# Kernel optimization log

Hardware: AMD Instinct MI355X
Metric: run time of the kernel (lower is better)

The kernel has to match this reference:

```python
import jax, jax.numpy as jnp
import numpy as np

B, T, E, H, V = 256, 32, 512, 512, 3000
SKIP = 2


def setup_inputs() -> dict:
    key = jax.random.key(0)
    ks = jax.random.split(key, 12)
    # sorted-descending ragged lengths, max forced to T (pack_padded_sequence requires descending)
    lengths = np.sort(np.asarray(jax.random.randint(ks[0], (B,), T // 2, T + 1)))[::-1].copy()
    lengths[0] = T
    s = 0.05
    return {
        "image_features": jax.random.normal(ks[1], (B, E // 2), jnp.float32),
        "text_features": jax.random.normal(ks[2], (B, E // 2), jnp.float32),
        "h0": jnp.zeros((B, H), jnp.float32),
        "c0": jnp.zeros((B, H), jnp.float32),
        "embed_table": jax.random.normal(ks[3], (V, E), jnp.float32) * 0.02,
        "W_ih": jax.random.normal(ks[4], (4 * H, E), jnp.float32) * s,
        "W_hh": jax.random.normal(ks[5], (4 * H, H), jnp.float32) * s,
        "b_ih": jnp.zeros((4 * H,), jnp.float32),
        "b_hh": jnp.zeros((4 * H,), jnp.float32),
        "W_out": jax.random.normal(ks[6], (V, 2 * H), jnp.float32) * s,
        "b_out": jnp.zeros((V,), jnp.float32),
        "answer": jax.random.randint(ks[7], (B, T), 0, V),
        "answer_lengths": lengths,  # numpy int array (static)
    }


def _lstm_cell(x, hx, cx, W_ih, W_hh, b_ih, b_hh):
    # torch.nn.LSTMCell math: gates ordered i, f, g, o
    g = x @ W_ih.T + b_ih + hx @ W_hh.T + b_hh
    i, f, gg, o = jnp.split(g, 4, axis=-1)
    cy = jax.nn.sigmoid(f) * cx + jax.nn.sigmoid(i) * jnp.tanh(gg)
    hy = jax.nn.sigmoid(o) * jnp.tanh(cy)
    return hy, cy


def _packed_indices(lengths, max_len, batch):
    # torch pack_padded_sequence (batch_first) ordering: for each timestep t,
    # rows 0..batch_sizes[t] of the (descending-sorted) batch, time-major concat.
    lengths = np.asarray(lengths)
    idx = np.concatenate([t * batch + np.arange(int((lengths > t).sum())) for t in range(max_len)])
    return jnp.asarray(idx)


def reference(image_features, text_features, h0, c0, embed_table,
              W_ih, W_hh, b_ih, b_hh, W_out, b_out, answer, answer_lengths):
    batch = image_features.shape[0]
    max_len = int(np.max(np.asarray(answer_lengths)))
    combined = jnp.concatenate([image_features, text_features], axis=1)  # [B, E]
    emb = embed_table[answer]                                            # [B, T, E]
    # inputs over time: step 0 = combined, steps 1..max_len-1 = embedded answer tokens
    xs = jnp.concatenate([combined[:, None, :], emb[:, : max_len - 1, :]], axis=1)
    xs = jnp.transpose(xs, (1, 0, 2))                                    # [T, B, E]
    ts = jnp.arange(max_len)

    def step(carry, inp):
        hx, cx, h_m2, h_m1, c_m2, c_m1 = carry
        t, x = inp
        hy, cy = _lstm_cell(x, hx, cx, W_ih, W_hh, b_ih, b_hh)
        # periodic skip-state residual: applied to the carried state AFTER storing hy/cy
        cond = (t >= SKIP) & (t % (SKIP + 1) == 0)
        hx_n = jnp.where(cond, hy + h_m2, hy)
        cx_n = jnp.where(cond, cy + c_m2, cy)
        return (hx_n, cx_n, h_m1, hy, c_m1, cy), (hy, cy)

    z = jnp.zeros_like(h0)
    (_, _, _, _, _, _), (hs, cs) = jax.lax.scan(step, (h0, c0, z, z, z, z), (ts, xs))
    results = jnp.concatenate([hs, cs], axis=-1)          # [T, B, 2H], time-major
    flat = results.reshape(max_len * batch, 2 * results.shape[-1] // 2)
    idx = _packed_indices(answer_lengths, max_len, batch)
    packed = flat[idx]                                    # [sum(lengths), 2H]
    return packed @ W_out.T + b_out                       # [sum(lengths), V]
```

## Files before the change

kernel.cpp:

```cpp
#include <hip/hip_runtime.h>
#include <hip/hip_bf16.h>

#define T_STEPS 32
#define BATCH 256
#define EDIM 512
#define HDIM 512
#define G4 2048
#define VOCAB 3000
#define VPAD 3072

#define NB_CVTW   8192
#define NB_WOUT   12288
#define NB_XS     16384
#define NB_CARRY  512

typedef short bf16x8 __attribute__((ext_vector_type(8)));
typedef float f32x4 __attribute__((ext_vector_type(4)));

__device__ __forceinline__ unsigned short f2b(float f){
  union { float f; unsigned int u; } x; x.f = f;
  unsigned int u = x.u;
  unsigned int r = (u + 0x7fffu + ((u >> 16) & 1u)) >> 16;
  return (unsigned short)r;
}
__device__ __forceinline__ float b2f(unsigned short h){
  union { unsigned int u; float f; } x; x.u = ((unsigned int)h) << 16;
  return x.f;
}
__device__ __forceinline__ float sigm(float x){ return 1.0f / (1.0f + expf(-x)); }

__device__ __forceinline__ void gload_lds16(const unsigned short* g, unsigned short* l){
  __builtin_amdgcn_global_load_lds(
      (const __attribute__((address_space(1))) unsigned int*)g,
      (__attribute__((address_space(3))) unsigned int*)l, 16, 0, 0);
}

__global__ __launch_bounds__(256) void k_prep(
    const float* __restrict__ wih, const float* __restrict__ whh,
    const float* __restrict__ wout,
    const float* __restrict__ img, const float* __restrict__ txt,
    const float* __restrict__ emb, const int* __restrict__ ans,
    const float* __restrict__ h0, const float* __restrict__ c0,
    const int* __restrict__ lengths,
    unsigned short* __restrict__ o_ih, unsigned short* __restrict__ o_hh,
    unsigned short* __restrict__ o_wo, unsigned short* __restrict__ xs,
    unsigned short* __restrict__ hx, float* __restrict__ cx,
    int* __restrict__ bs, int* __restrict__ roff, int* __restrict__ meta,
    int* __restrict__ rmap){
  int bid = blockIdx.x;
  if (bid < NB_CVTW){
    int i = bid * 256 + threadIdx.x;
    int n1 = G4 * EDIM;
    if (i < n1) o_ih[i] = f2b(wih[i]);
    else o_hh[i - n1] = f2b(whh[i - n1]);
    return;
  }
  bid -= NB_CVTW;
  if (bid < NB_WOUT){
    int i = bid * 256 + threadIdx.x;
    int r = i >> 10, c = i & 1023;
    o_wo[i] = (r < VOCAB) ? f2b(wout[r * 1024 + c]) : (unsigned short)0;
    return;
  }
  bid -= NB_WOUT;
  if (bid < NB_XS){
    int i = bid * 256 + threadIdx.x;
    int e = i & (EDIM - 1);
    int r = i >> 9;
    int t = r >> 8, b = r & 255;
    float v;
    if (t == 0) v = (e < 256) ? img[b * 256 + e] : txt[b * 256 + (e - 256)];
    else { int tok = ans[b * T_STEPS + (t - 1)]; v = emb[(size_t)tok * EDIM + e]; }
    xs[i] = f2b(v);
    return;
  }
  bid -= NB_XS;
  if (bid < NB_CARRY){
    int i = bid * 256 + threadIdx.x;
    hx[i] = f2b(h0[i]); cx[i] = c0[i];
    return;
  }
  {
    __shared__ int s[T_STEPS];
    __shared__ int sroff[T_STEPS + 1];
    int t = threadIdx.x;
    if (t < T_STEPS){
      int c = 0;
      for (int i = 0; i < BATCH; i++) c += (lengths[i] > t) ? 1 : 0;
      s[t] = c; bs[t] = c;
    }
    __syncthreads();
    if (t == 0){
      int acc = 0;
      for (int u = 0; u < T_STEPS; u++){ sroff[u] = acc; roff[u] = acc; acc += s[u]; }
      sroff[T_STEPS] = acc;
      meta[0] = acc;
    }
    __syncthreads();
    int ntot = sroff[T_STEPS];
    for (int r = t; r < T_STEPS * BATCH; r += 256){
      int tt = r >> 8, b = r & 255;
      if (b < s[tt]) rmap[sroff[tt] + b] = r;
    }
    for (int r = ntot + t; r < T_STEPS * BATCH; r += 256) rmap[r] = -1;
  }
}

template<int K>
__device__ __forceinline__ void gemm_tile(const unsigned short* __restrict__ A,
                                          const unsigned short* __restrict__ B,
                                          int row0, int col0,
                                          unsigned short* As, unsigned short* Bs,
                                          f32x4 acc[4][4]){
  const int tid = threadIdx.x, w = tid >> 6, l = tid & 63;
  const int la = l & 15, lkq = l >> 4;
  const int sr = l >> 3;
  const int ss = (l & 7) ^ sr;
  const int wr = (w >> 1) * 64, wc = (w & 1) * 64;
  const unsigned short* gA = A + (size_t)(row0 + w * 32 + sr) * K + ss * 8;
  const unsigned short* gB = B + (size_t)(col0 + w * 32 + sr) * K + ss * 8;
  unsigned short* lA = As + (w * 32) * 64;
  unsigned short* lB = Bs + (w * 32) * 64;
  for (int k0 = 0; k0 < K; k0 += 64){
#pragma unroll
    for (int i = 0; i < 4; i++){
      gload_lds16(gA + (size_t)i * 8 * K + k0, lA + i * 8 * 64);
      gload_lds16(gB + (size_t)i * 8 * K + k0, lB + i * 8 * 64);
    }
    __syncthreads();
#pragma unroll
    for (int kk = 0; kk < 2; kk++){
      bf16x8 a[4], b[4];
#pragma unroll
      for (int i = 0; i < 4; i++){
        int r = wr + i * 16 + la;
        a[i] = *(const bf16x8*)(As + r * 64 + (((kk * 4 + lkq) ^ (r & 7)) << 3));
      }
#pragma unroll
      for (int i = 0; i < 4; i++){
        int r = wc + i * 16 + la;
        b[i] = *(const bf16x8*)(Bs + r * 64 + (((kk * 4 + lkq) ^ (r & 7)) << 3));
      }
#pragma unroll
      for (int mi = 0; mi < 4; mi++)
#pragma unroll
        for (int ni = 0; ni < 4; ni++)
          acc[mi][ni] = __builtin_amdgcn_mfma_f32_16x16x32_bf16(a[mi], b[ni], acc[mi][ni], 0, 0, 0);
    }
    __syncthreads();
  }
}

__global__ __launch_bounds__(256) void k_gemm_xw(const unsigned short* __restrict__ A,
                                                 const unsigned short* __restrict__ W,
                                                 const float* __restrict__ bih,
                                                 const float* __restrict__ bhh,
                                                 unsigned short* __restrict__ C){
  __shared__ unsigned short As[128 * 64], Bs[128 * 64];
  int row0 = blockIdx.x * 128, col0 = blockIdx.y * 128;
  f32x4 acc[4][4] = {};
  gemm_tile<EDIM>(A, W, row0, col0, As, Bs, acc);
  int tid = threadIdx.x, w = tid >> 6, l = tid & 63;
  int la = l & 15, r4 = (l >> 4) * 4;
  int wr = (w >> 1) * 64, wc = (w & 1) * 64;
#pragma unroll
  for (int ni = 0; ni < 4; ni++){
    int col = col0 + wc + ni * 16 + la;
    float bias = bih[col] + bhh[col];
#pragma unroll
    for (int mi = 0; mi < 4; mi++)
#pragma unroll
      for (int j = 0; j < 4; j++){
        int row = row0 + wr + mi * 16 + r4 + j;
        C[(size_t)row * G4 + col] = f2b(acc[mi][ni][j] + bias);
      }
  }
}

__global__ __launch_bounds__(256, 2) void k_lstm_step(
    const unsigned short* __restrict__ XWt,
    const unsigned short* __restrict__ Whh,
    const unsigned short* __restrict__ hin,
    unsigned short* __restrict__ hout,
    float* __restrict__ cxio,
    unsigned short* __restrict__ hs_t,
    unsigned short* __restrict__ cs_t,
    const unsigned short* __restrict__ hs_m2,
    const unsigned short* __restrict__ cs_m2,
    int do_res){
  __shared__ unsigned short hA[16 * 512];
  __shared__ float gbuf[4][16][17];
  const int w = threadIdx.x >> 6, l = threadIdx.x & 63;
  const int la = l & 15, lkq = l >> 4;
  const int row0 = blockIdx.x * 16;
  const int hc0  = blockIdx.y * 16;
#pragma unroll
  for (int i = 0; i < 4; i++){
    int r = i * 4 + w;
    gload_lds16(hin + (size_t)(row0 + r) * HDIM + ((l ^ (r & 7)) << 3), hA + r * 512);
  }
  const unsigned short* Bp = Whh + (size_t)(w * HDIM + hc0 + la) * HDIM + lkq * 8;
  bf16x8 b[16];
#pragma unroll
  for (int kk = 0; kk < 16; kk++) b[kk] = *(const bf16x8*)(Bp + kk * 32);
  const int r4 = lkq * 4;
  float x[4];
#pragma unroll
  for (int j = 0; j < 4; j++)
    x[j] = b2f(XWt[(size_t)(row0 + r4 + j) * G4 + w * HDIM + hc0 + la]);
  __syncthreads();
  f32x4 acc = {};
#pragma unroll
  for (int kk = 0; kk < 16; kk++){
    bf16x8 a = *(const bf16x8*)(hA + la * 512 + (((kk * 4 + lkq) ^ (la & 7)) << 3));
    acc = __builtin_amdgcn_mfma_f32_16x16x32_bf16(a, b[kk], acc, 0, 0, 0);
  }
#pragma unroll
  for (int j = 0; j < 4; j++) gbuf[w][r4 + j][la] = acc[j] + x[j];
  __syncthreads();
  {
    int r = threadIdx.x >> 4, c = threadIdx.x & 15;
    size_t p = (size_t)(row0 + r) * HDIM + hc0 + c;
    float gi = gbuf[0][r][c], gf = gbuf[1][r][c], gg = gbuf[2][r][c], go = gbuf[3][r][c];
    float cprev = cxio[p];
    float cy = sigm(gf) * cprev + sigm(gi) * tanhf(gg);
    float hy = sigm(go) * tanhf(cy);
    hs_t[p] = f2b(hy);
    cs_t[p] = f2b(cy);
    float hn = hy, cn = cy;
    if (do_res){ hn += b2f(hs_m2[p]); cn += b2f(cs_m2[p]); }
    hout[p] = f2b(hn);
    cxio[p] = cn;
  }
}

__global__ __launch_bounds__(256) void k_gemm_out(const unsigned short* __restrict__ hs,
                                                  const unsigned short* __restrict__ cs,
                                                  const unsigned short* __restrict__ Wo,
                                                  const float* __restrict__ bout,
                                                  const int* __restrict__ meta,
                                                  const int* __restrict__ rmap,
                                                  float* __restrict__ out){
  int ntot = meta[0];
  int row0 = blockIdx.x * 128, col0 = blockIdx.y * 128;
  if (row0 >= ntot) return;
  __shared__ unsigned short As[128 * 64], Bs[128 * 64];
  const int tid = threadIdx.x, w = tid >> 6, l = tid & 63;
  const int la = l & 15, lkq = l >> 4;
  const int sr = l >> 3, ss = (l & 7) ^ sr;
  const int wr = (w >> 1) * 64, wc = (w & 1) * 64;
  int srow[4];
#pragma unroll
  for (int i = 0; i < 4; i++){
    int rr = rmap[row0 + w * 32 + sr + i * 8];
    srow[i] = rr < 0 ? 0 : rr;
  }
  const unsigned short* gB = Wo + (size_t)(col0 + w * 32 + sr) * 1024 + ss * 8;
  unsigned short* lA = As + (w * 32) * 64;
  unsigned short* lB = Bs + (w * 32) * 64;
  f32x4 acc[4][4] = {};
  for (int k0 = 0; k0 < 1024; k0 += 64){
#pragma unroll
    for (int i = 0; i < 4; i++){
      const unsigned short* srcA = (k0 < 512)
          ? hs + (size_t)srow[i] * 512 + k0 + ss * 8
          : cs + (size_t)srow[i] * 512 + (k0 - 512) + ss * 8;
      gload_lds16(srcA, lA + i * 8 * 64);
      gload_lds16(gB + (size_t)i * 8 * 1024 + k0, lB + i * 8 * 64);
    }
    __syncthreads();
#pragma unroll
    for (int kk = 0; kk < 2; kk++){
      bf16x8 a[4], b[4];
#pragma unroll
      for (int i = 0; i < 4; i++){
        int r = wr + i * 16 + la;
        a[i] = *(const bf16x8*)(As + r * 64 + (((kk * 4 + lkq) ^ (r & 7)) << 3));
      }
#pragma unroll
      for (int i = 0; i < 4; i++){
        int r = wc + i * 16 + la;
        b[i] = *(const bf16x8*)(Bs + r * 64 + (((kk * 4 + lkq) ^ (r & 7)) << 3));
      }
#pragma unroll
      for (int mi = 0; mi < 4; mi++)
#pragma unroll
        for (int ni = 0; ni < 4; ni++)
          acc[mi][ni] = __builtin_amdgcn_mfma_f32_16x16x32_bf16(a[mi], b[ni], acc[mi][ni], 0, 0, 0);
    }
    __syncthreads();
  }
  int r4 = (l >> 4) * 4;
#pragma unroll
  for (int ni = 0; ni < 4; ni++){
    int col = col0 + wc + ni * 16 + la;
    if (col >= VOCAB) continue;
    float bias = bout[col];
#pragma unroll
    for (int mi = 0; mi < 4; mi++)
#pragma unroll
      for (int j = 0; j < 4; j++){
        int row = row0 + wr + mi * 16 + r4 + j;
        if (row < ntot) out[(size_t)row * VOCAB + col] = acc[mi][ni][j] + bias;
      }
  }
}

extern "C" void kernel_launch(void* const* d_in, const int* in_sizes, int n_in,
                              void* d_out, int out_size, void* d_ws, size_t ws_size,
                              hipStream_t stream){
  const float* img   = (const float*)d_in[0];
  const float* txt   = (const float*)d_in[1];
  const float* h0    = (const float*)d_in[2];
  const float* c0    = (const float*)d_in[3];
  const float* emb   = (const float*)d_in[4];
  const float* W_ih  = (const float*)d_in[5];
  const float* W_hh  = (const float*)d_in[6];
  const float* b_ih  = (const float*)d_in[7];
  const float* b_hh  = (const float*)d_in[8];
  const float* W_out = (const float*)d_in[9];
  const float* b_out = (const float*)d_in[10];
  const int* answer  = (const int*)d_in[11];
  const int* lengths = (const int*)d_in[12];
  float* out = (float*)d_out;

  char* ws = (char*)d_ws;
  size_t off = 0;
  auto alloc = [&](size_t bytes) -> void* {
    void* p = ws + off; off += (bytes + 255) & ~(size_t)255; return p;
  };
  unsigned short* Wih_b = (unsigned short*)alloc((size_t)G4 * EDIM * 2);
  unsigned short* Whh_b = (unsigned short*)alloc((size_t)G4 * HDIM * 2);
  unsigned short* Wo_b  = (unsigned short*)alloc((size_t)VPAD * 1024 * 2);
  unsigned short* xs    = (unsigned short*)alloc((size_t)T_STEPS * BATCH * EDIM * 2);
  unsigned short* XW    = (unsigned short*)alloc((size_t)T_STEPS * BATCH * G4 * 2);
  unsigned short* hs    = (unsigned short*)alloc((size_t)T_STEPS * BATCH * HDIM * 2);
  unsigned short* cs    = (unsigned short*)alloc((size_t)T_STEPS * BATCH * HDIM * 2);
  unsigned short* hxA   = (unsigned short*)alloc((size_t)BATCH * HDIM * 2);
  unsigned short* hxB   = (unsigned short*)alloc((size_t)BATCH * HDIM * 2);
  float* cx             = (float*)alloc((size_t)BATCH * HDIM * 4);
  int* bsz  = (int*)alloc(T_STEPS * 4);
  int* roff = (int*)alloc(T_STEPS * 4);
  int* meta = (int*)alloc(256);
  int* rmap = (int*)alloc(T_STEPS * BATCH * 4);

  k_prep<<<dim3(NB_CVTW + NB_WOUT + NB_XS + NB_CARRY + 1), 256, 0, stream>>>(
      W_ih, W_hh, W_out, img, txt, emb, answer, h0, c0, lengths,
      Wih_b, Whh_b, Wo_b, xs, hxA, cx, bsz, roff, meta, rmap);

  k_gemm_xw<<<dim3(T_STEPS * BATCH / 128, G4 / 128), 256, 0, stream>>>(xs, Wih_b, b_ih, b_hh, XW);

  unsigned short* hbuf[2] = { hxA, hxB };
  for (int t = 0; t < T_STEPS; t++){
    int do_res = (t >= 2 && (t % 3) == 0) ? 1 : 0;
    int tm2 = (t >= 2) ? (t - 2) : 0;
    k_lstm_step<<<dim3(BATCH / 16, HDIM / 16), 256, 0, stream>>>(
        XW + (size_t)t * BATCH * G4, Whh_b, hbuf[t & 1], hbuf[(t + 1) & 1], cx,
        hs + (size_t)t * BATCH * HDIM, cs + (size_t)t * BATCH * HDIM,
        hs + (size_t)tm2 * BATCH * HDIM, cs + (size_t)tm2 * BATCH * HDIM, do_res);
  }

  k_gemm_out<<<dim3(T_STEPS * BATCH / 128, VPAD / 128), 256, 0, stream>>>(hs, cs, Wo_b, b_out, meta, rmap, out);
}
```

Before: 337.0 us.

## Split LSTM step K dimension across two wave groups with LDS reduction

The per-step LSTM kernel now runs 512 threads per block, with each of the four gate waves split into two halves that each handle half of the hidden K dimension. Partial MFMA results from the second half are reduced through shared memory before the gate nonlinearities. The aim is to halve per-wave serial MFMA and weight-load latency and raise parallelism on the latency-bound recurrent step. In exchange it adds an extra LDS round-trip and barrier, and half the threads sit idle in the elementwise tail.

Result: no change. 341.5 us (+1.3%).

```diff
diff --git a/kernel.cpp b/kernel.cpp
--- a/kernel.cpp
+++ b/kernel.cpp
@@ -177,7 +177,7 @@
   }
 }
 
-__global__ __launch_bounds__(256, 2) void k_lstm_step(
+__global__ __launch_bounds__(512, 4) void k_lstm_step(
     const unsigned short* __restrict__ XWt,
     const unsigned short* __restrict__ Whh,
     const unsigned short* __restrict__ hin,
@@ -189,37 +189,51 @@
     const unsigned short* __restrict__ cs_m2,
     int do_res){
   __shared__ unsigned short hA[16 * 512];
+  __shared__ float gbufP[4][16][17];
   __shared__ float gbuf[4][16][17];
-  const int w = threadIdx.x >> 6, l = threadIdx.x & 63;
+  const int tid = threadIdx.x;
+  const int w = tid >> 6, l = tid & 63;
+  const int g = w & 3, kh = w >> 2;
   const int la = l & 15, lkq = l >> 4;
   const int row0 = blockIdx.x * 16;
   const int hc0  = blockIdx.y * 16;
 #pragma unroll
-  for (int i = 0; i < 4; i++){
-    int r = i * 4 + w;
+  for (int i = 0; i < 2; i++){
+    int r = i * 8 + w;
     gload_lds16(hin + (size_t)(row0 + r) * HDIM + ((l ^ (r & 7)) << 3), hA + r * 512);
   }
-  const unsigned short* Bp = Whh + (size_t)(w * HDIM + hc0 + la) * HDIM + lkq * 8;
-  bf16x8 b[16];
-#pragma unroll
-  for (int kk = 0; kk < 16; kk++) b[kk] = *(const bf16x8*)(Bp + kk * 32);
+  const unsigned short* Bp = Whh + (size_t)(g * HDIM + hc0 + la) * HDIM + kh * 256 + lkq * 8;
+  bf16x8 b[8];
+#pragma unroll
+  for (int kk = 0; kk < 8; kk++) b[kk] = *(const bf16x8*)(Bp + kk * 32);
   const int r4 = lkq * 4;
-  float x[4];
-#pragma unroll
-  for (int j = 0; j < 4; j++)
-    x[j] = b2f(XWt[(size_t)(row0 + r4 + j) * G4 + w * HDIM + hc0 + la]);
+  float x[4] = {0.f, 0.f, 0.f, 0.f};
+  if (kh == 0){
+#pragma unroll
+    for (int j = 0; j < 4; j++)
+      x[j] = b2f(XWt[(size_t)(row0 + r4 + j) * G4 + g * HDIM + hc0 + la]);
+  }
   __syncthreads();
   f32x4 acc = {};
 #pragma unroll
-  for (int kk = 0; kk < 16; kk++){
-    bf16x8 a = *(const bf16x8*)(hA + la * 512 + (((kk * 4 + lkq) ^ (la & 7)) << 3));
+  for (int kk = 0; kk < 8; kk++){
+    int s = kh * 32 + kk * 4 + lkq;
+    bf16x8 a = *(const bf16x8*)(hA + la * 512 + ((s ^ (la & 7)) << 3));
     acc = __builtin_amdgcn_mfma_f32_16x16x32_bf16(a, b[kk], acc, 0, 0, 0);
   }
-#pragma unroll
-  for (int j = 0; j < 4; j++) gbuf[w][r4 + j][la] = acc[j] + x[j];
+  if (kh == 1){
+#pragma unroll
+    for (int j = 0; j < 4; j++) gbufP[g][r4 + j][la] = acc[j];
+  }
   __syncthreads();
-  {
-    int r = threadIdx.x >> 4, c = threadIdx.x & 15;
+  if (kh == 0){
+#pragma unroll
+    for (int j = 0; j < 4; j++)
+      gbuf[g][r4 + j][la] = acc[j] + gbufP[g][r4 + j][la] + x[j];
+  }
+  __syncthreads();
+  if (tid < 256){
+    int r = tid >> 4, c = tid & 15;
     size_t p = (size_t)(row0 + r) * HDIM + hc0 + c;
     float gi = gbuf[0][r][c], gf = gbuf[1][r][c], gg = gbuf[2][r][c], go = gbuf[3][r][c];
     float cprev = cxio[p];
@@ -354,7 +368,7 @@
   for (int t = 0; t < T_STEPS; t++){
     int do_res = (t >= 2 && (t % 3) == 0) ? 1 : 0;
     int tm2 = (t >= 2) ? (t - 2) : 0;
-    k_lstm_step<<<dim3(BATCH / 16, HDIM / 16), 256, 0, stream>>>(
+    k_lstm_step<<<dim3(BATCH / 16, HDIM / 16), 512, 0, stream>>>(
         XW + (size_t)t * BATCH * G4, Whh_b, hbuf[t & 1], hbuf[(t + 1) & 1], cx,
         hs + (size_t)t * BATCH * HDIM, cs + (size_t)t * BATCH * HDIM,
         hs + (size_t)tm2 * BATCH * HDIM, cs + (size_t)tm2 * BATCH * HDIM, do_res);
```

## Write packed h/c rows directly in LSTM step, drop gather map in output GEMM

Applied to the files above, without the earlier changes.

The LSTM step kernel now also writes each valid row's h and c into a contiguous packed [ntot, 1024] buffer at its packed-sequence offset. The output GEMM then reuses the generic gemm_tile on that packed matrix instead of gathering rows through an index map from separate hs/cs buffers. This removes the rmap construction in prep and the per-row indirection in the final GEMM. In exchange each step does extra scattered stores and the workspace grows by another activation-sized buffer.

After: 330.0 us. 2.1% less time.

```diff
diff --git a/kernel.cpp b/kernel.cpp
--- a/kernel.cpp
+++ b/kernel.cpp
@@ -45,8 +45,7 @@
     unsigned short* __restrict__ o_ih, unsigned short* __restrict__ o_hh,
     unsigned short* __restrict__ o_wo, unsigned short* __restrict__ xs,
     unsigned short* __restrict__ hx, float* __restrict__ cx,
-    int* __restrict__ bs, int* __restrict__ roff, int* __restrict__ meta,
-    int* __restrict__ rmap){
+    int* __restrict__ bs, int* __restrict__ roff, int* __restrict__ meta){
   int bid = blockIdx.x;
   if (bid < NB_CVTW){
     int i = bid * 256 + threadIdx.x;
@@ -82,7 +81,6 @@
   }
   {
     __shared__ int s[T_STEPS];
-    __shared__ int sroff[T_STEPS + 1];
     int t = threadIdx.x;
     if (t < T_STEPS){
       int c = 0;
@@ -92,17 +90,9 @@
     __syncthreads();
     if (t == 0){
       int acc = 0;
-      for (int u = 0; u < T_STEPS; u++){ sroff[u] = acc; roff[u] = acc; acc += s[u]; }
-      sroff[T_STEPS] = acc;
+      for (int u = 0; u < T_STEPS; u++){ roff[u] = acc; acc += s[u]; }
       meta[0] = acc;
     }
-    __syncthreads();
-    int ntot = sroff[T_STEPS];
-    for (int r = t; r < T_STEPS * BATCH; r += 256){
-      int tt = r >> 8, b = r & 255;
-      if (b < s[tt]) rmap[sroff[tt] + b] = r;
-    }
-    for (int r = ntot + t; r < T_STEPS * BATCH; r += 256) rmap[r] = -1;
   }
 }
 
@@ -187,13 +177,19 @@
     unsigned short* __restrict__ cs_t,
     const unsigned short* __restrict__ hs_m2,
     const unsigned short* __restrict__ cs_m2,
-    int do_res){
+    int do_res,
+    const int* __restrict__ bsp,
+    const int* __restrict__ roffp,
+    int t,
+    unsigned short* __restrict__ Apack){
   __shared__ unsigned short hA[16 * 512];
   __shared__ float gbuf[4][16][17];
   const int w = threadIdx.x >> 6, l = threadIdx.x & 63;
   const int la = l & 15, lkq = l >> 4;
   const int row0 = blockIdx.x * 16;
   const int hc0  = blockIdx.y * 16;
+  const int bs_t = bsp[t];
+  const int roff_t = roffp[t];
 #pragma unroll
   for (int i = 0; i < 4; i++){
     int r = i * 4 + w;
@@ -225,8 +221,14 @@
     float cprev = cxio[p];
     float cy = sigm(gf) * cprev + sigm(gi) * tanhf(gg);
     float hy = sigm(go) * tanhf(cy);
-    hs_t[p] = f2b(hy);
-    cs_t[p] = f2b(cy);
+    unsigned short hyb = f2b(hy), cyb = f2b(cy);
+    hs_t[p] = hyb;
+    cs_t[p] = cyb;
+    if (row0 + r < bs_t){
+      size_t pa = (size_t)(roff_t + row0 + r) * 1024 + hc0 + c;
+      Apack[pa] = hyb;
+      Apack[pa + 512] = cyb;
+    }
     float hn = hy, cn = cy;
     if (do_res){ hn += b2f(hs_m2[p]); cn += b2f(cs_m2[p]); }
     hout[p] = f2b(hn);
@@ -234,63 +236,20 @@
   }
 }
 
-__global__ __launch_bounds__(256) void k_gemm_out(const unsigned short* __restrict__ hs,
-                                                  const unsigned short* __restrict__ cs,
+__global__ __launch_bounds__(256) void k_gemm_out(const unsigned short* __restrict__ Ap,
                                                   const unsigned short* __restrict__ Wo,
                                                   const float* __restrict__ bout,
                                                   const int* __restrict__ meta,
-                                                  const int* __restrict__ rmap,
                                                   float* __restrict__ out){
   int ntot = meta[0];
   int row0 = blockIdx.x * 128, col0 = blockIdx.y * 128;
   if (row0 >= ntot) return;
   __shared__ unsigned short As[128 * 64], Bs[128 * 64];
-  const int tid = threadIdx.x, w = tid >> 6, l = tid & 63;
-  const int la = l & 15, lkq = l >> 4;
-  const int sr = l >> 3, ss = (l & 7) ^ sr;
-  const int wr = (w >> 1) * 64, wc = (w & 1) * 64;
-  int srow[4];
-#pragma unroll
-  for (int i = 0; i < 4; i++){
-    int rr = rmap[row0 + w * 32 + sr + i * 8];
-    srow[i] = rr < 0 ? 0 : rr;
-  }
-  const unsigned short* gB = Wo + (size_t)(col0 + w * 32 + sr) * 1024 + ss * 8;
-  unsigned short* lA = As + (w * 32) * 64;
-  unsigned short* lB = Bs + (w * 32) * 64;
   f32x4 acc[4][4] = {};
-  for (int k0 = 0; k0 < 1024; k0 += 64){
-#pragma unroll
-    for (int i = 0; i < 4; i++){
-      const unsigned short* srcA = (k0 < 512)
-          ? hs + (size_t)srow[i] * 512 + k0 + ss * 8
-          : cs + (size_t)srow[i] * 512 + (k0 - 512) + ss * 8;
-      gload_lds16(srcA, lA + i * 8 * 64);
-      gload_lds16(gB + (size_t)i * 8 * 1024 + k0, lB + i * 8 * 64);
-    }
-    __syncthreads();
-#pragma unroll
-    for (int kk = 0; kk < 2; kk++){
-      bf16x8 a[4], b[4];
-#pragma unroll
-      for (int i = 0; i < 4; i++){
-        int r = wr + i * 16 + la;
-        a[i] = *(const bf16x8*)(As + r * 64 + (((kk * 4 + lkq) ^ (r & 7)) << 3));
-      }
-#pragma unroll
-      for (int i = 0; i < 4; i++){
-        int r = wc + i * 16 + la;
-        b[i] = *(const bf16x8*)(Bs + r * 64 + (((kk * 4 + lkq) ^ (r & 7)) << 3));
-      }
-#pragma unroll
-      for (int mi = 0; mi < 4; mi++)
-#pragma unroll
-        for (int ni = 0; ni < 4; ni++)
-          acc[mi][ni] = __builtin_amdgcn_mfma_f32_16x16x32_bf16(a[mi], b[ni], acc[mi][ni], 0, 0, 0);
-    }
-    __syncthreads();
-  }
-  int r4 = (l >> 4) * 4;
+  gemm_tile<1024>(Ap, Wo, row0, col0, As, Bs, acc);
+  int tid = threadIdx.x, w = tid >> 6, l = tid & 63;
+  int la = l & 15, r4 = (l >> 4) * 4;
+  int wr = (w >> 1) * 64, wc = (w & 1) * 64;
 #pragma unroll
   for (int ni = 0; ni < 4; ni++){
     int col = col0 + wc + ni * 16 + la;
@@ -336,17 +295,17 @@
   unsigned short* XW    = (unsigned short*)alloc((size_t)T_STEPS * BATCH * G4 * 2);
   unsigned short* hs    = (unsigned short*)alloc((size_t)T_STEPS * BATCH * HDIM * 2);
   unsigned short* cs    = (unsigned short*)alloc((size_t)T_STEPS * BATCH * HDIM * 2);
+  unsigned short* Apack = (unsigned short*)alloc((size_t)T_STEPS * BATCH * 1024 * 2);
   unsigned short* hxA   = (unsigned short*)alloc((size_t)BATCH * HDIM * 2);
   unsigned short* hxB   = (unsigned short*)alloc((size_t)BATCH * HDIM * 2);
   float* cx             = (float*)alloc((size_t)BATCH * HDIM * 4);
   int* bsz  = (int*)alloc(T_STEPS * 4);
   int* roff = (int*)alloc(T_STEPS * 4);
   int* meta = (int*)alloc(256);
-  int* rmap = (int*)alloc(T_STEPS * BATCH * 4);
 
   k_prep<<<dim3(NB_CVTW + NB_WOUT + NB_XS + NB_CARRY + 1), 256, 0, stream>>>(
       W_ih, W_hh, W_out, img, txt, emb, answer, h0, c0, lengths,
-      Wih_b, Whh_b, Wo_b, xs, hxA, cx, bsz, roff, meta, rmap);
+      Wih_b, Whh_b, Wo_b, xs, hxA, cx, bsz, roff, meta);
 
   k_gemm_xw<<<dim3(T_STEPS * BATCH / 128, G4 / 128), 256, 0, stream>>>(xs, Wih_b, b_ih, b_hh, XW);
 
@@ -357,8 +316,9 @@
     k_lstm_step<<<dim3(BATCH / 16, HDIM / 16), 256, 0, stream>>>(
         XW + (size_t)t * BATCH * G4, Whh_b, hbuf[t & 1], hbuf[(t + 1) & 1], cx,
         hs + (size_t)t * BATCH * HDIM, cs + (size_t)t * BATCH * HDIM,
-        hs + (size_t)tm2 * BATCH * HDIM, cs + (size_t)tm2 * BATCH * HDIM, do_res);
-  }
-
-  k_gemm_out<<<dim3(T_STEPS * BATCH / 128, VPAD / 128), 256, 0, stream>>>(hs, cs, Wo_b, b_out, meta, rmap, out);
-}
+        hs + (size_t)tm2 * BATCH * HDIM, cs + (size_t)tm2 * BATCH * HDIM, do_res,
+        bsz, roff, t, Apack);
+  }
+
+  k_gemm_out<<<dim3(T_STEPS * BATCH / 128, VPAD / 128), 256, 0, stream>>>(Apack, Wo_b, b_out, meta, out);
+}
```
